# Optimization experiments

Hardware: AMD Instinct MI355X
Metric: run time of the kernel (lower is better)

## Reference

```python
import jax, jax.numpy as jnp
import numpy as np

NUM_HEADS = 16
INPUT_DIM = 1024
ATTENTION_DIM = 1024
DEPTH = ATTENTION_DIM // NUM_HEADS
NEG = -(2.0 ** 32) + 1.0  # large negative used by the original masking


def setup_inputs() -> dict:
    key = jax.random.key(0)
    kq, kk, k1, k2, k3 = jax.random.split(key, 5)
    B, L = 4, 1024
    s = 1.0 / np.sqrt(INPUT_DIM)
    return {
        "query": jax.random.normal(kq, (B, L, INPUT_DIM), dtype=jnp.float32),
        "key": jax.random.normal(kk, (B, L, INPUT_DIM), dtype=jnp.float32),
        "Wq": jax.random.normal(k1, (INPUT_DIM, ATTENTION_DIM), dtype=jnp.float32) * s,
        "Wk": jax.random.normal(k2, (INPUT_DIM, ATTENTION_DIM), dtype=jnp.float32) * s,
        "Wv": jax.random.normal(k3, (INPUT_DIM, ATTENTION_DIM), dtype=jnp.float32) * s,
    }


def reference(query, key, Wq, Wk, Wv):
    B, Lq, _ = query.shape
    Lk = key.shape[1]
    q = query @ Wq  # [B, Lq, A]
    k = key @ Wk    # [B, Lk, A]
    v = key @ Wv
    # Faithful to torch: raw row-major reshape [B, L, A] -> [B*H, L, depth]
    q_ = q.reshape(-1, Lq, DEPTH)
    k_ = k.reshape(-1, Lk, DEPTH)
    v_ = v.reshape(-1, Lk, DEPTH)
    scores = jnp.einsum('bid,bjd->bij', q_, k_) / (DEPTH ** 0.5)  # [BH, Lq, Lk]
    # key padding mask, tiled head-major like torch.tile(key_mask, [H, 1])
    key_mask = jnp.sign(jnp.abs(key.sum(-1)))           # [B, Lk]
    key_mask = jnp.tile(key_mask, (NUM_HEADS, 1))        # [HB, Lk]
    scores = jnp.where(key_mask[:, None, :] == 0, NEG, scores)
    # causal mask
    tril = jnp.tril(jnp.ones((Lq, Lk), dtype=scores.dtype))
    scores = jnp.where(tril[None] == 0, NEG, scores)
    attn = jax.nn.softmax(scores, axis=-1)
    # query mask: original tiles to [HB, Lk, Lq] and multiplies elementwise,
    # i.e. masks the LAST axis with the query mask (requires Lq == Lk)
    query_mask = jnp.sign(jnp.abs(query.sum(-1)))        # [B, Lq]
    query_mask = jnp.tile(query_mask, (NUM_HEADS, 1))    # [HB, Lq]
    attn = attn * query_mask[:, None, :]
    # dropout is identity in eval mode
    out = attn @ v_                                      # [BH, Lq, depth]
    out = jnp.concatenate(jnp.split(out, NUM_HEADS, axis=0), axis=-1)  # [B, Lq, A]
    out = out + query
    norm = jnp.sqrt(jnp.sum(out * out, axis=-1, keepdims=True))
    out = out / jnp.maximum(norm, 1e-12)
    return out
```

## Files before the change

kernel.cpp:

```cpp
#include <hip/hip_runtime.h>
#include <cstdint>
#include <cstddef>


#define US unsigned short

typedef __attribute__((ext_vector_type(4))) float f32x4;
typedef __attribute__((ext_vector_type(8))) short bf16x8;
typedef __attribute__((ext_vector_type(8))) US ushort8_t;
typedef __attribute__((ext_vector_type(4))) US ushort4_t;

__device__ __forceinline__ US f2bf(float f) {
  union { float f; uint32_t u; } c; c.f = f;
  uint32_t u = c.u;
  return (US)((u + 0x7FFFu + ((u >> 16) & 1u)) >> 16);
}

__device__ __forceinline__ uint32_t cvtpk(float lo, float hi) {
  uint32_t r;
  asm("v_cvt_pk_bf16_f32 %0, %1, %2" : "=v"(r) : "v"(lo), "v"(hi));
  return r;
}

__device__ __forceinline__ void gld16(const void* g, void* l) {
  __builtin_amdgcn_global_load_lds(
      (const __attribute__((address_space(1))) uint32_t*)g,
      (__attribute__((address_space(3))) uint32_t*)l, 16, 0, 0);
}

__global__ __launch_bounds__(256) void cvt2bf(const float* __restrict__ q,
                                              const float* __restrict__ k,
                                              US* __restrict__ qb,
                                              US* __restrict__ kb) {
  uint32_t i = blockIdx.x * 256u + threadIdx.x;
  const bool isq = i < 1048576u;
  const float4* src = (const float4*)(isq ? q : k);
  US* dst = isq ? qb : kb;
  uint32_t j = isq ? i : i - 1048576u;
  float4 v = src[j];
  ushort4_t o = { f2bf(v.x), f2bf(v.y), f2bf(v.z), f2bf(v.w) };
  *(ushort4_t*)(dst + (size_t)j * 4) = o;
}

__global__ __launch_bounds__(256) void wtrans(const float* __restrict__ Wq,
                                              const float* __restrict__ Wk,
                                              const float* __restrict__ Wv,
                                              US* __restrict__ Tq,
                                              US* __restrict__ Tk,
                                              US* __restrict__ Tv) {
  const int z = blockIdx.z;
  const float* W = (z == 0) ? Wq : (z == 1) ? Wk : Wv;
  US* T = (z == 0) ? Tq : (z == 1) ? Tk : Tv;
  __shared__ float tile[64][65];
  const int r0 = blockIdx.x * 64, c0 = blockIdx.y * 64;
  const int tx = threadIdx.x & 63, ty = threadIdx.x >> 6;
  #pragma unroll
  for (int rr = ty; rr < 64; rr += 4)
    tile[rr][tx] = W[(size_t)(r0 + rr) * 1024 + c0 + tx];
  __syncthreads();
  #pragma unroll
  for (int rr = ty; rr < 64; rr += 4)
    T[(size_t)(c0 + rr) * 1024 + r0 + tx] = f2bf(tile[tx][rr]);
}

__global__ __launch_bounds__(256) void gemm_qkv(
    const US* __restrict__ qin, const US* __restrict__ kin,
    const US* __restrict__ WqT, const US* __restrict__ WkT,
    const US* __restrict__ WvT,
    US* __restrict__ qo, US* __restrict__ ko, US* __restrict__ vo) {
  const int z = blockIdx.z;
  const US* A = (z == 0) ? qin : kin;
  const US* B = (z == 0) ? WqT : (z == 1) ? WkT : WvT;
  US* C = (z == 0) ? qo : (z == 1) ? ko : vo;

  __shared__ __align__(16) US Abuf[128 * 32];
  __shared__ __align__(16) US Bbuf[128 * 32];

  const int t = threadIdx.x;
  const int w = t >> 6, l = t & 63;
  const int lr = l & 15, lu = l >> 4;
  const int brow = blockIdx.x * 128;
  const int bcol = blockIdx.y * 128;
  const int wm = (w >> 1) * 64, wn = (w & 1) * 64;

  f32x4 acc[4][4] = {};

  for (int ks = 0; ks < 32; ++ks) {
    const int kb = ks * 32;
    #pragma unroll
    for (int qq = 0; qq < 2; ++qq) {
      const int s = (qq * 4 + w) * 64 + l;
      const int r = s >> 2;
      const int cs = (l & 3) ^ (r & 3);
      gld16(A + (size_t)(brow + r) * 1024 + kb + cs * 8,
            (char*)Abuf + (qq * 4 + w) * 1024);
      gld16(B + (size_t)(bcol + r) * 1024 + kb + cs * 8,
            (char*)Bbuf + (qq * 4 + w) * 1024);
    }
    __syncthreads();

    bf16x8 af[4], bfr[4];
    #pragma unroll
    for (int mf = 0; mf < 4; ++mf) {
      const int ra = wm + mf * 16 + lr;
      af[mf] = *(const bf16x8*)((const char*)Abuf + ra * 64 + ((lu ^ (ra & 3)) * 16));
      const int rb = wn + mf * 16 + lr;
      bfr[mf] = *(const bf16x8*)((const char*)Bbuf + rb * 64 + ((lu ^ (rb & 3)) * 16));
    }
    #pragma unroll
    for (int mf = 0; mf < 4; ++mf)
      #pragma unroll
      for (int nf = 0; nf < 4; ++nf)
        acc[mf][nf] = __builtin_amdgcn_mfma_f32_16x16x32_bf16(af[mf], bfr[nf],
                                                              acc[mf][nf], 0, 0, 0);
    __syncthreads();
  }

  #pragma unroll
  for (int mf = 0; mf < 4; ++mf)
    #pragma unroll
    for (int nf = 0; nf < 4; ++nf)
      #pragma unroll
      for (int i = 0; i < 4; ++i) {
        const int row = brow + wm + mf * 16 + lu * 4 + i;
        const int col = bcol + wn + nf * 16 + lr;
        C[(size_t)row * 1024 + col] = f2bf(acc[mf][nf][i]);
      }
}

__global__ __launch_bounds__(256) void vtrans(const US* __restrict__ v,
                                              US* __restrict__ vT) {
  const int g = blockIdx.x;
  const int kt = blockIdx.y;
  __shared__ __align__(16) US tile[64][72];
  const US* src = v + (size_t)g * 65536;
  US* dst = vT + (size_t)g * 65536;
  const int t = threadIdx.x;
  #pragma unroll
  for (int q = 0; q < 2; ++q) {
    const int s = q * 256 + t;
    const int key = s >> 3, dc = (s & 7) * 8;
    *(ushort8_t*)&tile[key][dc] =
        *(const ushort8_t*)(src + (size_t)(kt * 64 + key) * 64 + dc);
  }
  __syncthreads();
  #pragma unroll
  for (int i = 0; i < 16; ++i) {
    const int idx = i * 256 + t;
    const int d = idx >> 6, kl = idx & 63;
    dst[(size_t)d * 1024 + kt * 64 + kl] = tile[kl][d];
  }
}

__global__ __launch_bounds__(512, 4) void attn(const US* __restrict__ qbf,
                                               const US* __restrict__ kbf,
                                               const US* __restrict__ vT,
                                               float* __restrict__ ab) {
  const int x = blockIdx.x;
  const int g = x & 63;
  const int idx = x >> 6;
  const int s = (idx < 4) ? (7 - idx) : (idx - 4);
  const int w = threadIdx.x >> 6, l = threadIdx.x & 63;
  const int lr = l & 15, lu = l >> 4;
  const int i0 = s * 128 + w * 16;

  const US* Qg = qbf + (size_t)g * 65536;
  const US* Kg = kbf + (size_t)g * 65536;
  const US* Vg = vT + (size_t)g * 65536;

  __shared__ __align__(16) US Kt[2][64][64];
  __shared__ __align__(16) US Vt[2][64][64];
  __shared__ __align__(16) US Plds[8][16][72];

  bf16x8 qf[2];
  #pragma unroll
  for (int kc = 0; kc < 2; ++kc)
    qf[kc] = *(const bf16x8*)(Qg + (size_t)(i0 + lr) * 64 + kc * 32 + lu * 8);

  f32x4 o[4] = {};
  float lsp = 0.f;
  const float SC = 0.18033688011112042f;
  const float CB = 5.770780163555852f;

  const int ns_blk = 2 * s + 2;
  const int my_ns  = (i0 + 79) >> 6;

  const int srow = w * 8 + (l >> 3);
  const int sunit = (l & 7) ^ (srow & 7);
  auto stage = [&](int buf, int jb) {
    gld16(Kg + (size_t)(jb + srow) * 64 + sunit * 8, (char*)Kt[buf] + w * 1024);
    gld16(Vg + (size_t)srow * 1024 + jb + sunit * 8, (char*)Vt[buf] + w * 1024);
  };

  stage(0, 0);
  __syncthreads();

  for (int jt = 0; jt < ns_blk; ++jt) {
    const int buf = jt & 1;
    if (jt + 1 < ns_blk) stage(buf ^ 1, (jt + 1) * 64);

    if (jt < my_ns) {
      const int jb = jt * 64;
      f32x4 s4[4] = {};
      #pragma unroll
      for (int nt = 0; nt < 4; ++nt) {
        const int row = nt * 16 + lr;
        #pragma unroll
        for (int kc = 0; kc < 2; ++kc) {
          bf16x8 kf = *(const bf16x8*)((const char*)Kt[buf] + row * 128 +
                                       (((kc * 4 + lu) ^ (lr & 7)) * 16));
          s4[nt] = __builtin_amdgcn_mfma_f32_16x16x32_bf16(kf, qf[kc], s4[nt], 0, 0, 0);
        }
      }
      const int tdiag = i0 + lr - jb;
      #pragma unroll
      for (int nt = 0; nt < 4; ++nt) {
        float e[4];
        #pragma unroll
        for (int r = 0; r < 4; ++r) {
          float arg = s4[nt][r] * SC - CB;
          if (nt * 16 + lu * 4 + r > tdiag) arg = -__builtin_inff();
          e[r] = __builtin_amdgcn_exp2f(arg);
          lsp += e[r];
        }
        uint2 wv;
        wv.x = cvtpk(e[0], e[1]);
        wv.y = cvtpk(e[2], e[3]);
        *(uint2*)&Plds[w][lr][nt * 16 + lu * 4] = wv;
      }
      #pragma unroll
      for (int c = 0; c < 2; ++c) {
        bf16x8 pf = *(const bf16x8*)&Plds[w][lr][c * 32 + lu * 8];
        #pragma unroll
        for (int dt = 0; dt < 4; ++dt) {
          const int vrow = dt * 16 + lr;
          bf16x8 vf = *(const bf16x8*)((const char*)Vt[buf] + vrow * 128 +
                                       (((c * 4 + lu) ^ (lr & 7)) * 16));
          o[dt] = __builtin_amdgcn_mfma_f32_16x16x32_bf16(vf, pf, o[dt], 0, 0, 0);
        }
      }
    }
    __syncthreads();
  }

  float ls = lsp;
  ls += __shfl_xor(ls, 16);
  ls += __shfl_xor(ls, 32);
  const float inv = 1.0f / ls;
  const int i = i0 + lr;
  const size_t base = (size_t)(g & 3) * 1048576 + (size_t)i * 1024 + (g >> 2) * 64;
  #pragma unroll
  for (int dt = 0; dt < 4; ++dt) {
    f32x4 ov = o[dt] * inv;
    *(f32x4*)(ab + base + dt * 16 + lu * 4) = ov;
  }
}

__global__ __launch_bounds__(256) void epi(const float* __restrict__ ab,
                                           const float* __restrict__ query,
                                           float* __restrict__ out) {
  const int row = blockIdx.x;
  const int t = threadIdx.x;
  const float4 x = ((const float4*)(ab + (size_t)row * 1024))[t];
  const float4 y = ((const float4*)(query + (size_t)row * 1024))[t];
  float4 v;
  v.x = x.x + y.x; v.y = x.y + y.y; v.z = x.z + y.z; v.w = x.w + y.w;
  float ss = v.x * v.x + v.y * v.y + v.z * v.z + v.w * v.w;
  #pragma unroll
  for (int d = 1; d < 64; d <<= 1) ss += __shfl_xor(ss, d, 64);
  __shared__ float red[4];
  if ((t & 63) == 0) red[t >> 6] = ss;
  __syncthreads();
  const float tot = red[0] + red[1] + red[2] + red[3];
  const float inv = 1.0f / fmaxf(sqrtf(tot), 1e-12f);
  float4 o2;
  o2.x = v.x * inv; o2.y = v.y * inv; o2.z = v.z * inv; o2.w = v.w * inv;
  ((float4*)(out + (size_t)row * 1024))[t] = o2;
}

extern "C" void kernel_launch(void* const* d_in, const int* in_sizes, int n_in,
                              void* d_out, int out_size, void* d_ws, size_t ws_size,
                              hipStream_t stream) {
  const float* query = (const float*)d_in[0];
  const float* key   = (const float*)d_in[1];
  const float* Wq    = (const float*)d_in[2];
  const float* Wk    = (const float*)d_in[3];
  const float* Wv    = (const float*)d_in[4];
  float* out = (float*)d_out;

  char* ws = (char*)d_ws;
  const size_t MB = 1u << 20;
  US* query_bf = (US*)(ws + 0);
  US* key_bf   = (US*)(ws + 8 * MB);
  US* WqT = (US*)(ws + 16 * MB);
  US* WkT = (US*)(ws + 18 * MB);
  US* WvT = (US*)(ws + 20 * MB);
  US* q_bf = (US*)(ws + 22 * MB);
  US* k_bf = (US*)(ws + 30 * MB);
  US* v_bf = (US*)(ws + 38 * MB);
  US* vTb  = (US*)(ws + 46 * MB);
  float* ab = (float*)(ws + 0);

  cvt2bf<<<8192, 256, 0, stream>>>(query, key, query_bf, key_bf);
  wtrans<<<dim3(16, 16, 3), 256, 0, stream>>>(Wq, Wk, Wv, WqT, WkT, WvT);
  gemm_qkv<<<dim3(32, 8, 3), 256, 0, stream>>>(query_bf, key_bf, WqT, WkT, WvT,
                                               q_bf, k_bf, v_bf);
  vtrans<<<dim3(64, 16), 256, 0, stream>>>(v_bf, vTb);
  attn<<<512, 512, 0, stream>>>(q_bf, k_bf, vTb, ab);
  epi<<<4096, 256, 0, stream>>>(ab, query, out);
}
```

Baseline: 91.50 us.

## Merge conversion kernels, widen GEMM K-tile to 64, add MFMA priority hints

Folds the input-conversion and weight-transpose kernels into one launch to save a kernel launch. Doubles the QKV GEMM K-step from 32 to 64 with an 8-way XOR swizzle, halving the number of barrier-separated iterations. Adds s_setprio around the MFMA blocks in the GEMM and attention kernels so matrix work gets scheduling priority. The larger K-tile doubles LDS use per block, which could lower occupancy.

```diff
diff --git a/kernel.cpp b/kernel.cpp
--- a/kernel.cpp
+++ b/kernel.cpp
@@ -28,31 +28,35 @@
       (__attribute__((address_space(3))) uint32_t*)l, 16, 0, 0);
 }
 
-__global__ __launch_bounds__(256) void cvt2bf(const float* __restrict__ q,
-                                              const float* __restrict__ k,
-                                              US* __restrict__ qb,
-                                              US* __restrict__ kb) {
-  uint32_t i = blockIdx.x * 256u + threadIdx.x;
-  const bool isq = i < 1048576u;
-  const float4* src = (const float4*)(isq ? q : k);
-  US* dst = isq ? qb : kb;
-  uint32_t j = isq ? i : i - 1048576u;
-  float4 v = src[j];
-  ushort4_t o = { f2bf(v.x), f2bf(v.y), f2bf(v.z), f2bf(v.w) };
-  *(ushort4_t*)(dst + (size_t)j * 4) = o;
-}
-
-__global__ __launch_bounds__(256) void wtrans(const float* __restrict__ Wq,
-                                              const float* __restrict__ Wk,
-                                              const float* __restrict__ Wv,
-                                              US* __restrict__ Tq,
-                                              US* __restrict__ Tk,
-                                              US* __restrict__ Tv) {
-  const int z = blockIdx.z;
+__global__ __launch_bounds__(256) void prep(const float* __restrict__ q,
+                                            const float* __restrict__ k,
+                                            US* __restrict__ qb,
+                                            US* __restrict__ kb,
+                                            const float* __restrict__ Wq,
+                                            const float* __restrict__ Wk,
+                                            const float* __restrict__ Wv,
+                                            US* __restrict__ Tq,
+                                            US* __restrict__ Tk,
+                                            US* __restrict__ Tv) {
+  const int bid = blockIdx.x;
+  if (bid < 8192) {
+    uint32_t i = bid * 256u + threadIdx.x;
+    const bool isq = i < 1048576u;
+    const float4* src = (const float4*)(isq ? q : k);
+    US* dst = isq ? qb : kb;
+    uint32_t j = isq ? i : i - 1048576u;
+    float4 v = src[j];
+    ushort4_t o = { f2bf(v.x), f2bf(v.y), f2bf(v.z), f2bf(v.w) };
+    *(ushort4_t*)(dst + (size_t)j * 4) = o;
+    return;
+  }
+  const int rem = bid - 8192;
+  const int z = rem >> 8;
+  const int r8 = rem & 255;
   const float* W = (z == 0) ? Wq : (z == 1) ? Wk : Wv;
   US* T = (z == 0) ? Tq : (z == 1) ? Tk : Tv;
   __shared__ float tile[64][65];
-  const int r0 = blockIdx.x * 64, c0 = blockIdx.y * 64;
+  const int r0 = (r8 >> 4) * 64, c0 = (r8 & 15) * 64;
   const int tx = threadIdx.x & 63, ty = threadIdx.x >> 6;
   #pragma unroll
   for (int rr = ty; rr < 64; rr += 4)
@@ -73,8 +77,8 @@
   const US* B = (z == 0) ? WqT : (z == 1) ? WkT : WvT;
   US* C = (z == 0) ? qo : (z == 1) ? ko : vo;
 
-  __shared__ __align__(16) US Abuf[128 * 32];
-  __shared__ __align__(16) US Bbuf[128 * 32];
+  __shared__ __align__(16) US Abuf[128 * 64];
+  __shared__ __align__(16) US Bbuf[128 * 64];
 
   const int t = threadIdx.x;
   const int w = t >> 6, l = t & 63;
@@ -85,34 +89,40 @@
 
   f32x4 acc[4][4] = {};
 
-  for (int ks = 0; ks < 32; ++ks) {
-    const int kb = ks * 32;
+  for (int ks = 0; ks < 16; ++ks) {
+    const int kb = ks * 64;
     #pragma unroll
-    for (int qq = 0; qq < 2; ++qq) {
-      const int s = (qq * 4 + w) * 64 + l;
-      const int r = s >> 2;
-      const int cs = (l & 3) ^ (r & 3);
-      gld16(A + (size_t)(brow + r) * 1024 + kb + cs * 8,
-            (char*)Abuf + (qq * 4 + w) * 1024);
-      gld16(B + (size_t)(bcol + r) * 1024 + kb + cs * 8,
-            (char*)Bbuf + (qq * 4 + w) * 1024);
+    for (int rd = 0; rd < 4; ++rd) {
+      const int s = rd * 256 + t;
+      const int r = s >> 3;
+      const int u = (l & 7) ^ (r & 7);
+      const size_t lofs = (size_t)(rd * 256 + w * 64) * 16;
+      gld16(A + (size_t)(brow + r) * 1024 + kb + u * 8, (char*)Abuf + lofs);
+      gld16(B + (size_t)(bcol + r) * 1024 + kb + u * 8, (char*)Bbuf + lofs);
     }
     __syncthreads();
 
-    bf16x8 af[4], bfr[4];
     #pragma unroll
-    for (int mf = 0; mf < 4; ++mf) {
-      const int ra = wm + mf * 16 + lr;
-      af[mf] = *(const bf16x8*)((const char*)Abuf + ra * 64 + ((lu ^ (ra & 3)) * 16));
-      const int rb = wn + mf * 16 + lr;
-      bfr[mf] = *(const bf16x8*)((const char*)Bbuf + rb * 64 + ((lu ^ (rb & 3)) * 16));
+    for (int kk = 0; kk < 2; ++kk) {
+      bf16x8 af[4], bfr[4];
+      #pragma unroll
+      for (int mf = 0; mf < 4; ++mf) {
+        const int ra = wm + mf * 16 + lr;
+        af[mf] = *(const bf16x8*)((const char*)Abuf + ra * 128 +
+                                  (((kk * 4 + lu) ^ (ra & 7)) * 16));
+        const int rb = wn + mf * 16 + lr;
+        bfr[mf] = *(const bf16x8*)((const char*)Bbuf + rb * 128 +
+                                   (((kk * 4 + lu) ^ (rb & 7)) * 16));
+      }
+      __builtin_amdgcn_s_setprio(1);
+      #pragma unroll
+      for (int mf = 0; mf < 4; ++mf)
+        #pragma unroll
+        for (int nf = 0; nf < 4; ++nf)
+          acc[mf][nf] = __builtin_amdgcn_mfma_f32_16x16x32_bf16(af[mf], bfr[nf],
+                                                                acc[mf][nf], 0, 0, 0);
+      __builtin_amdgcn_s_setprio(0);
     }
-    #pragma unroll
-    for (int mf = 0; mf < 4; ++mf)
-      #pragma unroll
-      for (int nf = 0; nf < 4; ++nf)
-        acc[mf][nf] = __builtin_amdgcn_mfma_f32_16x16x32_bf16(af[mf], bfr[nf],
-                                                              acc[mf][nf], 0, 0, 0);
     __syncthreads();
   }
 
@@ -231,6 +241,7 @@
       #pragma unroll
       for (int c = 0; c < 2; ++c) {
         bf16x8 pf = *(const bf16x8*)&Plds[w][lr][c * 32 + lu * 8];
+        __builtin_amdgcn_s_setprio(1);
         #pragma unroll
         for (int dt = 0; dt < 4; ++dt) {
           const int vrow = dt * 16 + lr;
@@ -238,6 +249,7 @@
                                        (((c * 4 + lu) ^ (lr & 7)) * 16));
           o[dt] = __builtin_amdgcn_mfma_f32_16x16x32_bf16(vf, pf, o[dt], 0, 0, 0);
         }
+        __builtin_amdgcn_s_setprio(0);
       }
     }
     __syncthreads();
@@ -301,8 +313,8 @@
   US* vTb  = (US*)(ws + 46 * MB);
   float* ab = (float*)(ws + 0);
 
-  cvt2bf<<<8192, 256, 0, stream>>>(query, key, query_bf, key_bf);
-  wtrans<<<dim3(16, 16, 3), 256, 0, stream>>>(Wq, Wk, Wv, WqT, WkT, WvT);
+  prep<<<8960, 256, 0, stream>>>(query, key, query_bf, key_bf,
+                                 Wq, Wk, Wv, WqT, WkT, WvT);
   gemm_qkv<<<dim3(32, 8, 3), 256, 0, stream>>>(query_bf, key_bf, WqT, WkT, WvT,
                                                q_bf, k_bf, v_bf);
   vtrans<<<dim3(64, 16), 256, 0, stream>>>(v_bf, vTb);
```

Result: faster. 81.87 us (-10.5%).
